# Optimization experiments

Measured on AMD Instinct MI355X. Metric: run time of the kernel, lower is better.

The kernel has to match this reference:

```python
import jax, jax.numpy as jnp
import numpy as np

EPS = 1e-5

def layer_norm(x, gamma, beta):
    mu = jnp.mean(x, axis=-1, keepdims=True)
    var = jnp.var(x, axis=-1, keepdims=True)
    return (x - mu) * jax.lax.rsqrt(var + EPS) * gamma + beta

def setup_inputs() -> dict:
    key = jax.random.key(0)
    ks = jax.random.split(key, 8)
    T, B, E, H, K = 2048, 2, 1024, 16, 64
    x = jax.random.normal(ks[0], (T, B, E), dtype=jnp.float32)
    # causal mask: 0 where allowed (s<=t), -1e9 where masked
    attn_mask = jnp.where(jnp.tril(jnp.ones((T, T), dtype=bool)), 0.0, -1e9).astype(jnp.float32)
    def xavier(k, shape, gain):
        fan_out, fan_in = shape
        std = gain * np.sqrt(2.0 / (fan_in + fan_out))
        return (jax.random.normal(k, shape, dtype=jnp.float32) * std)
    Wq = xavier(ks[1], (H * K, E), 1.0)
    Wk = xavier(ks[2], (K, E), 1.0)
    Wv = xavier(ks[3], (E, E), 1.0)
    return {
        'x': x, 'attn_mask': attn_mask,
        'Wq': Wq, 'bq': jnp.zeros((H * K,), jnp.float32),
        'Wk': Wk, 'bk': jnp.zeros((K,), jnp.float32),
        'Wv': Wv, 'bv': jnp.zeros((E,), jnp.float32),
        'k_gamma': jnp.ones((K,), jnp.float32), 'k_beta': jnp.zeros((K,), jnp.float32),
        'v_gamma': jnp.ones((E,), jnp.float32), 'v_beta': jnp.zeros((E,), jnp.float32),
    }

def reference(x, attn_mask, Wq, bq, Wk, bk, Wv, bv, k_gamma, k_beta, v_gamma, v_beta):
    T, B, E = x.shape
    K = Wk.shape[0]
    H = Wq.shape[0] // K
    q = (x @ Wq.T + bq).reshape(T, B, H, K)          # [T,B,H,K]
    k = layer_norm(x @ Wk.T + bk, k_gamma, k_beta)   # [T,B,K]
    v = layer_norm(x @ Wv.T + bv, v_gamma, v_beta)   # [T,B,E]
    # outer-product state per step, then causal cumulative sum.
    # einsum('ts,sbkd->tbkd', scaling*causal_mask, s) == cumsum over s<=t,
    # scaled per query position t by (t+1)^-0.5 (mask is causal lower-tri).
    outer = jnp.einsum('tbk,tbd->tbkd', k, v)        # [T,B,K,E]
    s = jnp.cumsum(outer, axis=0)
    scaling = jax.lax.rsqrt(jnp.arange(1, T + 1, dtype=x.dtype))
    s = s * scaling[:, None, None, None]
    qn = jnp.mean(jax.nn.softmax(q, axis=-1), axis=2)  # [T,B,K] (dropout_p=0, eval)
    attn = jnp.einsum('tbk,tbkd->tbd', qn, s)          # [T,B,E]
    return attn
```

## Files before the change

### kernel.cpp

```cpp
#include <hip/hip_runtime.h>
#include <math.h>

#define T_DIM 2048
#define B_DIM 2
#define E_DIM 1024
#define K_DIM 64
#define H_DIM 16
#define R_DIM (T_DIM * B_DIM)
#define WROWS 2176
#define NTILE 136

typedef __bf16 bf16x8 __attribute__((ext_vector_type(8)));
typedef __bf16 bf16x4 __attribute__((ext_vector_type(4)));
typedef float f32x4 __attribute__((ext_vector_type(4)));

#define GLD16(gptr, lptr)                                                      \
    __builtin_amdgcn_global_load_lds(                                          \
        (const __attribute__((address_space(1))) void*)(gptr),                 \
        (__attribute__((address_space(3))) void*)(lptr), 16, 0, 0)

__global__ __launch_bounds__(256) void cvt_all(const float* __restrict__ X,
                                               const float* __restrict__ Wq,
                                               const float* __restrict__ Wv,
                                               const float* __restrict__ Wk,
                                               __bf16* __restrict__ XB,
                                               __bf16* __restrict__ WB) {
    const size_t nq = (size_t)1024 * 1024;
    const size_t nk = (size_t)64 * 1024;
    bf16x8 o;
    if (blockIdx.x < 2048) {
        size_t g = ((size_t)blockIdx.x * 256 + threadIdx.x) * 8;
        float4 a = *(const float4*)&X[g];
        float4 b = *(const float4*)&X[g + 4];
        o[0] = (__bf16)a.x; o[1] = (__bf16)a.y; o[2] = (__bf16)a.z; o[3] = (__bf16)a.w;
        o[4] = (__bf16)b.x; o[5] = (__bf16)b.y; o[6] = (__bf16)b.z; o[7] = (__bf16)b.w;
        *(bf16x8*)&XB[g] = o;
    } else {
        size_t g = ((size_t)(blockIdx.x - 2048) * 256 + threadIdx.x) * 8;
        if (g < 2 * nq + nk) {
            const float* src;
            size_t off;
            if (g < nq)          { src = Wq; off = g; }
            else if (g < 2 * nq) { src = Wv; off = g - nq; }
            else                 { src = Wk; off = g - 2 * nq; }
            float4 a = *(const float4*)&src[off];
            float4 b = *(const float4*)&src[off + 4];
            o[0] = (__bf16)a.x; o[1] = (__bf16)a.y; o[2] = (__bf16)a.z; o[3] = (__bf16)a.w;
            o[4] = (__bf16)b.x; o[5] = (__bf16)b.y; o[6] = (__bf16)b.z; o[7] = (__bf16)b.w;
        } else {
#pragma unroll
            for (int i = 0; i < 8; ++i) o[i] = (__bf16)0.f;
        }
        *(bf16x8*)&WB[g] = o;
    }
}

__global__ __launch_bounds__(256) void gemm_mfma(const __bf16* __restrict__ XB,
                                                 const __bf16* __restrict__ WB,
                                                 const float* __restrict__ bq,
                                                 const float* __restrict__ bv,
                                                 const float* __restrict__ bk,
                                                 __bf16* __restrict__ Qb,
                                                 __bf16* __restrict__ Vb,
                                                 float* __restrict__ Kr) {
    __shared__ __bf16 Als[128 * 32];
    __shared__ __bf16 Bls[128 * 32];
    const int tid = threadIdx.x;
    const int lane = tid & 63;
    const int w = tid >> 6;
    const int wm = (w & 1) * 64;
    const int wn = (w >> 1) * 64;
    const int rBase = blockIdx.x * 128;
    const int cBase = blockIdx.y * 128;

    const int c0 = tid, c1 = tid + 256;
    const __bf16* gA0 = XB + (size_t)(rBase + (c0 >> 2)) * E_DIM + (c0 & 3) * 8;
    const __bf16* gA1 = XB + (size_t)(rBase + (c1 >> 2)) * E_DIM + (c1 & 3) * 8;
    const __bf16* gB0 = WB + (size_t)(cBase + (c0 >> 2)) * E_DIM + (c0 & 3) * 8;
    const __bf16* gB1 = WB + (size_t)(cBase + (c1 >> 2)) * E_DIM + (c1 & 3) * 8;
    __bf16* lA0 = Als + c0 * 8;
    __bf16* lA1 = Als + c1 * 8;
    __bf16* lB0 = Bls + c0 * 8;
    __bf16* lB1 = Bls + c1 * 8;

    const int fr = lane & 15;
    const int fk = (lane >> 4) * 8;
    const __bf16* aF = Als + (wm + fr) * 32 + fk;
    const __bf16* bF = Bls + (wn + fr) * 32 + fk;

    f32x4 acc[4][4] = {};

    for (int kk = 0; kk < E_DIM; kk += 32) {
        __syncthreads();
        GLD16(gA0 + kk, lA0);
        GLD16(gA1 + kk, lA1);
        GLD16(gB0 + kk, lB0);
        GLD16(gB1 + kk, lB1);
        __syncthreads();

        bf16x8 af[4], bfr[4];
#pragma unroll
        for (int mt = 0; mt < 4; ++mt) af[mt] = *(const bf16x8*)(aF + mt * 16 * 32);
#pragma unroll
        for (int nt = 0; nt < 4; ++nt) bfr[nt] = *(const bf16x8*)(bF + nt * 16 * 32);
#pragma unroll
        for (int mt = 0; mt < 4; ++mt)
#pragma unroll
            for (int nt = 0; nt < 4; ++nt)
                acc[mt][nt] = __builtin_amdgcn_mfma_f32_16x16x32_bf16(
                    af[mt], bfr[nt], acc[mt][nt], 0, 0, 0);
    }

    const int row0 = rBase + wm + (lane >> 4) * 4;
    if (cBase < 2048) {
        const float* bias;
        __bf16* Cout;
        int colBase;
        if (cBase < 1024) { bias = bq; Cout = Qb; colBase = cBase; }
        else              { bias = bv; Cout = Vb; colBase = cBase - 1024; }
        const int col0 = colBase + wn + (lane & 15);
#pragma unroll
        for (int mt = 0; mt < 4; ++mt)
#pragma unroll
            for (int nt = 0; nt < 4; ++nt) {
                int cc = col0 + nt * 16;
                float bb = bias[cc];
#pragma unroll
                for (int r = 0; r < 4; ++r)
                    Cout[(size_t)(row0 + mt * 16 + r) * E_DIM + cc] =
                        (__bf16)(acc[mt][nt][r] + bb);
            }
    } else {
        const int col0 = wn + (lane & 15);
#pragma unroll
        for (int mt = 0; mt < 4; ++mt)
#pragma unroll
            for (int nt = 0; nt < 4; ++nt) {
                int cc = col0 + nt * 16;
                if (cc < 64) {
                    float bb = bk[cc];
#pragma unroll
                    for (int r = 0; r < 4; ++r)
                        Kr[(size_t)(row0 + mt * 16 + r) * K_DIM + cc] =
                            acc[mt][nt][r] + bb;
                }
            }
    }
}

__global__ __launch_bounds__(256) void rowops(const __bf16* __restrict__ Qb,
                                              const float* __restrict__ Kraw,
                                              const __bf16* __restrict__ Vb,
                                              const float* __restrict__ kg,
                                              const float* __restrict__ kb,
                                              __bf16* __restrict__ QNB,
                                              __bf16* __restrict__ KNB,
                                              float2* __restrict__ ST) {
    const int r = blockIdx.x;
    const int tid = threadIdx.x;
    const int lane = tid & 63, wv = tid >> 6;
    const int t = r >> 1, b = r & 1;
    __shared__ float redq[4][64];
    __shared__ float redv[2][4];

    float acc = 0.f;
#pragma unroll
    for (int h4 = 0; h4 < 4; ++h4) {
        int h = wv * 4 + h4;
        float v = (float)Qb[(size_t)r * 1024 + h * 64 + lane];
        float m = v;
#pragma unroll
        for (int off = 32; off; off >>= 1) m = fmaxf(m, __shfl_xor(m, off));
        float e = expf(v - m);
        float ssum = e;
#pragma unroll
        for (int off = 32; off; off >>= 1) ssum += __shfl_xor(ssum, off);
        acc += e / ssum;
    }
    redq[wv][lane] = acc;

    {
        bf16x4 v4 = *(const bf16x4*)&Vb[(size_t)r * 1024 + tid * 4];
        float a = (float)v4[0], c = (float)v4[1], d = (float)v4[2], e = (float)v4[3];
        float s = a + c + d + e;
        float s2 = a * a + c * c + d * d + e * e;
#pragma unroll
        for (int off = 32; off; off >>= 1) {
            s += __shfl_xor(s, off);
            s2 += __shfl_xor(s2, off);
        }
        if (lane == 0) { redv[0][wv] = s; redv[1][wv] = s2; }
    }
    __syncthreads();

    if (tid < 64) {
        float s = redq[0][tid] + redq[1][tid] + redq[2][tid] + redq[3][tid];
        QNB[((size_t)b * T_DIM + t) * K_DIM + tid] = (__bf16)(s * (1.f / 16.f));
    } else if (tid < 128) {
        float v = Kraw[(size_t)r * K_DIM + lane];
        float s = v, s2 = v * v;
#pragma unroll
        for (int off = 32; off; off >>= 1) {
            s += __shfl_xor(s, off);
            s2 += __shfl_xor(s2, off);
        }
        float mean = s * (1.f / 64.f);
        float var = s2 * (1.f / 64.f) - mean * mean;
        float inv = rsqrtf(var + 1e-5f);
        KNB[((size_t)b * T_DIM + t) * K_DIM + lane] =
            (__bf16)((v - mean) * inv * kg[lane] + kb[lane]);
    } else if (tid == 128) {
        float s = redv[0][0] + redv[0][1] + redv[0][2] + redv[0][3];
        float s2 = redv[1][0] + redv[1][1] + redv[1][2] + redv[1][3];
        float mean = s * (1.f / 1024.f);
        float var = s2 * (1.f / 1024.f) - mean * mean;
        ST[r] = make_float2(mean, rsqrtf(var + 1e-5f));
    }
}

__global__ __launch_bounds__(256) void prep_score(const __bf16* __restrict__ VB,
                                                  const float2* __restrict__ ST,
                                                  const float* __restrict__ gamma,
                                                  const float* __restrict__ beta,
                                                  __bf16* __restrict__ VT,
                                                  const __bf16* __restrict__ QNB,
                                                  const __bf16* __restrict__ KNB,
                                                  __bf16* __restrict__ Pg) {
    __shared__ __align__(16) unsigned char smem[36864];
    const int bid = blockIdx.x;
    const int tid = threadIdx.x;

    if (bid < 1024) {
        float (*tile)[65] = (float(*)[65])smem;
        const int tb = bid & 31, eb = (bid >> 5) & 15, b = bid >> 9;
#pragma unroll
        for (int j = 0; j < 2; ++j) {
            int idx = tid + j * 256;
            int tl = idx >> 3, e8 = idx & 7;
            int r = (tb * 64 + tl) * B_DIM + b;
            float2 st = ST[r];
            bf16x8 v = *(const bf16x8*)&VB[(size_t)r * E_DIM + eb * 64 + e8 * 8];
#pragma unroll
            for (int i = 0; i < 8; ++i)
                tile[tl][e8 * 8 + i] = ((float)v[i] - st.x) * st.y;
        }
        __syncthreads();
#pragma unroll
        for (int j = 0; j < 4; ++j) {
            int idx = tid + j * 256;
            int e = idx >> 4, t4 = idx & 15;
            float g = gamma[eb * 64 + e], bb = beta[eb * 64 + e];
            bf16x4 o;
#pragma unroll
            for (int i = 0; i < 4; ++i) o[i] = (__bf16)(tile[t4 * 4 + i][e] * g + bb);
            *(bf16x4*)&VT[((size_t)b * E_DIM + eb * 64 + e) * T_DIM + tb * 64 + t4 * 4] = o;
        }
    } else {
        __bf16* qns = (__bf16*)smem;
        __bf16* kns = (__bf16*)(smem + 18432);
        const int idx0 = bid - 1024;
        const int b = idx0 & 1;
        const int tileId = idx0 >> 1;
        int qt = 0, rem = tileId;
        while (rem > qt) { rem -= (qt + 1); ++qt; }
        const int st = rem;
        const int lane = tid & 63;
        const int w = tid >> 6;
        const int qL = lane & 15;
        const int quad = lane >> 4;

        const __bf16* qsrc = QNB + ((size_t)b * T_DIM + qt * 128) * K_DIM;
        const __bf16* ksrc = KNB + ((size_t)b * T_DIM + st * 128) * K_DIM;
#pragma unroll
        for (int j = 0; j < 4; ++j) {
            int idx = tid + j * 256;
            int row = idx >> 3, k8 = idx & 7;
            *(bf16x8*)&qns[row * 72 + k8 * 8] = *(const bf16x8*)&qsrc[row * K_DIM + k8 * 8];
            *(bf16x8*)&kns[row * 72 + k8 * 8] = *(const bf16x8*)&ksrc[row * K_DIM + k8 * 8];
        }
        __syncthreads();

        f32x4 acc[8][2] = {};
#pragma unroll
        for (int kit = 0; kit < 2; ++kit) {
            bf16x8 bfr[2];
#pragma unroll
            for (int nt = 0; nt < 2; ++nt) {
                int q = w * 32 + nt * 16 + qL;
                bfr[nt] = *(const bf16x8*)&qns[q * 72 + kit * 32 + quad * 8];
            }
#pragma unroll
            for (int mt = 0; mt < 8; ++mt) {
                bf16x8 af = *(const bf16x8*)&kns[(mt * 16 + qL) * 72 + kit * 32 + quad * 8];
#pragma unroll
                for (int nt = 0; nt < 2; ++nt)
                    acc[mt][nt] = __builtin_amdgcn_mfma_f32_16x16x32_bf16(
                        af, bfr[nt], acc[mt][nt], 0, 0, 0);
            }
        }
        __bf16* pb = Pg + ((size_t)(b * NTILE + tileId)) * 128 * 128;
#pragma unroll
        for (int mt = 0; mt < 8; ++mt)
#pragma unroll
            for (int nt = 0; nt < 2; ++nt) {
                int q = w * 32 + nt * 16 + qL;
                int s0 = mt * 16 + quad * 4;
                bf16x4 o;
#pragma unroll
                for (int r = 0; r < 4; ++r) {
                    float val = acc[mt][nt][r];
                    if (qt == st && (s0 + r) > q) val = 0.f;
                    o[r] = (__bf16)val;
                }
                *(bf16x4*)&pb[(size_t)q * 128 + s0] = o;
            }
    }
}

__global__ __launch_bounds__(256) void flashPV(const __bf16* __restrict__ Pg,
                                               const __bf16* __restrict__ VT,
                                               float* __restrict__ OUT) {
    __shared__ __align__(16) __bf16 vts[64 * 136];
    __shared__ __align__(16) __bf16 ps[128 * 136];
    const int p = blockIdx.x;
    const int es = blockIdx.y;
    const int b = blockIdx.z;
    const int tid = threadIdx.x;
    const int lane = tid & 63;
    const int w = tid >> 6;
    const int qL = lane & 15;
    const int quad = lane >> 4;

    for (int ph = 0; ph < 2; ++ph) {
        const int qt = ph ? (15 - p) : p;
        const int tileBase = qt * (qt + 1) / 2;
        f32x4 acc[4][2] = {};

        for (int st = 0; st <= qt; ++st) {
            __syncthreads();
#pragma unroll
            for (int j = 0; j < 4; ++j) {
                int idx = tid + j * 256;
                int e = idx >> 4, sc = idx & 15;
                *(bf16x8*)&vts[e * 136 + sc * 8] =
                    *(const bf16x8*)&VT[((size_t)b * E_DIM + es * 64 + e) * T_DIM +
                                        st * 128 + sc * 8];
            }
            const __bf16* pb = Pg + ((size_t)(b * NTILE + tileBase + st)) * 128 * 128;
#pragma unroll
            for (int j = 0; j < 8; ++j) {
                int idx = tid + j * 256;
                int q = idx >> 4, sc = idx & 15;
                *(bf16x8*)&ps[q * 136 + sc * 8] = *(const bf16x8*)&pb[q * 128 + sc * 8];
            }
            __syncthreads();
#pragma unroll
            for (int kit = 0; kit < 4; ++kit) {
                bf16x8 bfr[2];
#pragma unroll
                for (int nt = 0; nt < 2; ++nt) {
                    int q = w * 32 + nt * 16 + qL;
                    bfr[nt] = *(const bf16x8*)&ps[q * 136 + kit * 32 + quad * 8];
                }
#pragma unroll
                for (int mt = 0; mt < 4; ++mt) {
                    bf16x8 af = *(const bf16x8*)&vts[(mt * 16 + qL) * 136 + kit * 32 + quad * 8];
#pragma unroll
                    for (int nt = 0; nt < 2; ++nt)
                        acc[mt][nt] = __builtin_amdgcn_mfma_f32_16x16x32_bf16(
                            af, bfr[nt], acc[mt][nt], 0, 0, 0);
                }
            }
        }
        __syncthreads();

        float* tb = (float*)vts + w * 640;
#pragma unroll
        for (int mt = 0; mt < 4; ++mt) {
#pragma unroll
            for (int nt = 0; nt < 2; ++nt)
                *(f32x4*)&tb[(nt * 16 + qL) * 20 + quad * 4] = acc[mt][nt];
#pragma unroll
            for (int j = 0; j < 2; ++j) {
                int fid = lane + j * 64;
                int q = fid >> 2, e4 = fid & 3;
                float4 val = *(const float4*)&tb[q * 20 + e4 * 4];
                int t = qt * 128 + w * 32 + q;
                float sca = rsqrtf((float)(t + 1));
                float4 r = {val.x * sca, val.y * sca, val.z * sca, val.w * sca};
                *(float4*)&OUT[((size_t)t * B_DIM + b) * E_DIM + es * 64 + mt * 16 + e4 * 4] = r;
            }
        }
    }
}

extern "C" void kernel_launch(void* const* d_in, const int* in_sizes, int n_in,
                              void* d_out, int out_size, void* d_ws,
                              size_t ws_size, hipStream_t stream) {
    const float* x = (const float*)d_in[0];
    const float* Wq = (const float*)d_in[2];
    const float* bq = (const float*)d_in[3];
    const float* Wk = (const float*)d_in[4];
    const float* bk = (const float*)d_in[5];
    const float* Wv = (const float*)d_in[6];
    const float* bv = (const float*)d_in[7];
    const float* kg = (const float*)d_in[8];
    const float* kb = (const float*)d_in[9];
    const float* vg = (const float*)d_in[10];
    const float* vb = (const float*)d_in[11];
    float* out = (float*)d_out;

    char* base = (char*)d_ws;
    const size_t MB = 1024 * 1024;
    __bf16* qb    = (__bf16*)(base + 0);
    __bf16* vbuf  = (__bf16*)(base + 8 * MB);
    float*  kraw  = (float*)(base + 16 * MB);
    __bf16* xb    = (__bf16*)(base + 17 * MB);
    __bf16* wb    = (__bf16*)(base + 25 * MB);
    __bf16* qnb   = (__bf16*)(base + 30 * MB);
    __bf16* knb   = (__bf16*)(base + 31 * MB);
    float2* stats = (float2*)(base + 32 * MB);
    __bf16* Pg  = (__bf16*)(base + 0);
    __bf16* vbT = xb;

    cvt_all<<<dim3(2048 + WROWS * 1024 / 2048), 256, 0, stream>>>(x, Wq, Wv, Wk, xb, wb);
    gemm_mfma<<<dim3(32, 17), 256, 0, stream>>>(xb, wb, bq, bv, bk, qb, vbuf, kraw);
    rowops<<<dim3(R_DIM), 256, 0, stream>>>(qb, kraw, vbuf, kg, kb, qnb, knb, stats);
    prep_score<<<dim3(1024 + 2 * NTILE), 256, 0, stream>>>(vbuf, stats, vg, vb, vbT,
                                                           qnb, knb, Pg);
    flashPV<<<dim3(8, 16, B_DIM), 256, 0, stream>>>(Pg, vbT, out);
}
```

Measured before the change: 183.6 us.

## Double-buffer GEMM LDS loads and split flashPV query-tile pairs across blocks

The projection GEMM now uses two LDS buffers, so the async global-to-LDS loads for the next k-slice are issued before computing the current one, leaving one barrier per step instead of two. flashPV no longer pairs tiles p and 15-p inside a single block. It launches one block per query tile (16×16×2 blocks), issued longest-first to improve parallelism and load balance. Risks include doubled LDS use in the GEMM, which may lower occupancy, and whether the loads actually overlap given the synchronization pattern.

```diff
diff --git a/kernel.cpp b/kernel.cpp
--- a/kernel.cpp
+++ b/kernel.cpp
@@ -63,8 +63,8 @@
                                                  __bf16* __restrict__ Qb,
                                                  __bf16* __restrict__ Vb,
                                                  float* __restrict__ Kr) {
-    __shared__ __bf16 Als[128 * 32];
-    __shared__ __bf16 Bls[128 * 32];
+    __shared__ __bf16 Als[2][128 * 32];
+    __shared__ __bf16 Bls[2][128 * 32];
     const int tid = threadIdx.x;
     const int lane = tid & 63;
     const int w = tid >> 6;
@@ -78,38 +78,61 @@
     const __bf16* gA1 = XB + (size_t)(rBase + (c1 >> 2)) * E_DIM + (c1 & 3) * 8;
     const __bf16* gB0 = WB + (size_t)(cBase + (c0 >> 2)) * E_DIM + (c0 & 3) * 8;
     const __bf16* gB1 = WB + (size_t)(cBase + (c1 >> 2)) * E_DIM + (c1 & 3) * 8;
-    __bf16* lA0 = Als + c0 * 8;
-    __bf16* lA1 = Als + c1 * 8;
-    __bf16* lB0 = Bls + c0 * 8;
-    __bf16* lB1 = Bls + c1 * 8;
+    __bf16* lA0_0 = &Als[0][c0 * 8];
+    __bf16* lA1_0 = &Als[0][c1 * 8];
+    __bf16* lB0_0 = &Bls[0][c0 * 8];
+    __bf16* lB1_0 = &Bls[0][c1 * 8];
+    __bf16* lA0_1 = &Als[1][c0 * 8];
+    __bf16* lA1_1 = &Als[1][c1 * 8];
+    __bf16* lB0_1 = &Bls[1][c0 * 8];
+    __bf16* lB1_1 = &Bls[1][c1 * 8];
 
     const int fr = lane & 15;
     const int fk = (lane >> 4) * 8;
-    const __bf16* aF = Als + (wm + fr) * 32 + fk;
-    const __bf16* bF = Bls + (wn + fr) * 32 + fk;
+    const __bf16* aF_0 = &Als[0][(wm + fr) * 32 + fk];
+    const __bf16* bF_0 = &Bls[0][(wn + fr) * 32 + fk];
+    const __bf16* aF_1 = &Als[1][(wm + fr) * 32 + fk];
+    const __bf16* bF_1 = &Bls[1][(wn + fr) * 32 + fk];
 
     f32x4 acc[4][4] = {};
 
-    for (int kk = 0; kk < E_DIM; kk += 32) {
-        __syncthreads();
-        GLD16(gA0 + kk, lA0);
-        GLD16(gA1 + kk, lA1);
-        GLD16(gB0 + kk, lB0);
-        GLD16(gB1 + kk, lB1);
-        __syncthreads();
-
-        bf16x8 af[4], bfr[4];
-#pragma unroll
-        for (int mt = 0; mt < 4; ++mt) af[mt] = *(const bf16x8*)(aF + mt * 16 * 32);
-#pragma unroll
-        for (int nt = 0; nt < 4; ++nt) bfr[nt] = *(const bf16x8*)(bF + nt * 16 * 32);
-#pragma unroll
-        for (int mt = 0; mt < 4; ++mt)
-#pragma unroll
-            for (int nt = 0; nt < 4; ++nt)
-                acc[mt][nt] = __builtin_amdgcn_mfma_f32_16x16x32_bf16(
-                    af[mt], bfr[nt], acc[mt][nt], 0, 0, 0);
-    }
+#define STAGE(B, KK)                                                           \
+    {                                                                          \
+        GLD16(gA0 + (KK), lA0_##B);                                            \
+        GLD16(gA1 + (KK), lA1_##B);                                            \
+        GLD16(gB0 + (KK), lB0_##B);                                            \
+        GLD16(gB1 + (KK), lB1_##B);                                            \
+    }
+#define COMPUTE(B)                                                             \
+    {                                                                          \
+        bf16x8 af[4], bfr[4];                                                  \
+        _Pragma("unroll") for (int mt = 0; mt < 4; ++mt)                       \
+            af[mt] = *(const bf16x8*)(aF_##B + mt * 16 * 32);                  \
+        _Pragma("unroll") for (int nt = 0; nt < 4; ++nt)                       \
+            bfr[nt] = *(const bf16x8*)(bF_##B + nt * 16 * 32);                 \
+        _Pragma("unroll") for (int mt = 0; mt < 4; ++mt)                       \
+            _Pragma("unroll") for (int nt = 0; nt < 4; ++nt)                   \
+                acc[mt][nt] = __builtin_amdgcn_mfma_f32_16x16x32_bf16(         \
+                    af[mt], bfr[nt], acc[mt][nt], 0, 0, 0);                    \
+    }
+
+    STAGE(0, 0);
+    __syncthreads();
+    STAGE(1, 32);
+    COMPUTE(0);
+    __syncthreads();
+    for (int kk = 64; kk < E_DIM; kk += 64) {
+        STAGE(0, kk);
+        COMPUTE(1);
+        __syncthreads();
+        STAGE(1, kk + 32);
+        COMPUTE(0);
+        __syncthreads();
+    }
+    COMPUTE(1);
+
+#undef STAGE
+#undef COMPUTE
 
     const int row0 = rBase + wm + (lane >> 4) * 4;
     if (cBase < 2048) {
@@ -322,7 +345,7 @@
                                                float* __restrict__ OUT) {
     __shared__ __align__(16) __bf16 vts[64 * 136];
     __shared__ __align__(16) __bf16 ps[128 * 136];
-    const int p = blockIdx.x;
+    const int qt = 15 - (int)blockIdx.x;
     const int es = blockIdx.y;
     const int b = blockIdx.z;
     const int tid = threadIdx.x;
@@ -331,65 +354,62 @@
     const int qL = lane & 15;
     const int quad = lane >> 4;
 
-    for (int ph = 0; ph < 2; ++ph) {
-        const int qt = ph ? (15 - p) : p;
-        const int tileBase = qt * (qt + 1) / 2;
-        f32x4 acc[4][2] = {};
-
-        for (int st = 0; st <= qt; ++st) {
-            __syncthreads();
-#pragma unroll
-            for (int j = 0; j < 4; ++j) {
-                int idx = tid + j * 256;
-                int e = idx >> 4, sc = idx & 15;
-                *(bf16x8*)&vts[e * 136 + sc * 8] =
-                    *(const bf16x8*)&VT[((size_t)b * E_DIM + es * 64 + e) * T_DIM +
-                                        st * 128 + sc * 8];
-            }
-            const __bf16* pb = Pg + ((size_t)(b * NTILE + tileBase + st)) * 128 * 128;
-#pragma unroll
-            for (int j = 0; j < 8; ++j) {
-                int idx = tid + j * 256;
-                int q = idx >> 4, sc = idx & 15;
-                *(bf16x8*)&ps[q * 136 + sc * 8] = *(const bf16x8*)&pb[q * 128 + sc * 8];
-            }
-            __syncthreads();
-#pragma unroll
-            for (int kit = 0; kit < 4; ++kit) {
-                bf16x8 bfr[2];
-#pragma unroll
-                for (int nt = 0; nt < 2; ++nt) {
-                    int q = w * 32 + nt * 16 + qL;
-                    bfr[nt] = *(const bf16x8*)&ps[q * 136 + kit * 32 + quad * 8];
-                }
-#pragma unroll
-                for (int mt = 0; mt < 4; ++mt) {
-                    bf16x8 af = *(const bf16x8*)&vts[(mt * 16 + qL) * 136 + kit * 32 + quad * 8];
-#pragma unroll
-                    for (int nt = 0; nt < 2; ++nt)
-                        acc[mt][nt] = __builtin_amdgcn_mfma_f32_16x16x32_bf16(
-                            af, bfr[nt], acc[mt][nt], 0, 0, 0);
-                }
-            }
-        }
-        __syncthreads();
-
-        float* tb = (float*)vts + w * 640;
-#pragma unroll
-        for (int mt = 0; mt < 4; ++mt) {
-#pragma unroll
-            for (int nt = 0; nt < 2; ++nt)
-                *(f32x4*)&tb[(nt * 16 + qL) * 20 + quad * 4] = acc[mt][nt];
-#pragma unroll
-            for (int j = 0; j < 2; ++j) {
-                int fid = lane + j * 64;
-                int q = fid >> 2, e4 = fid & 3;
-                float4 val = *(const float4*)&tb[q * 20 + e4 * 4];
-                int t = qt * 128 + w * 32 + q;
-                float sca = rsqrtf((float)(t + 1));
-                float4 r = {val.x * sca, val.y * sca, val.z * sca, val.w * sca};
-                *(float4*)&OUT[((size_t)t * B_DIM + b) * E_DIM + es * 64 + mt * 16 + e4 * 4] = r;
-            }
+    const int tileBase = qt * (qt + 1) / 2;
+    f32x4 acc[4][2] = {};
+
+    for (int st = 0; st <= qt; ++st) {
+        __syncthreads();
+#pragma unroll
+        for (int j = 0; j < 4; ++j) {
+            int idx = tid + j * 256;
+            int e = idx >> 4, sc = idx & 15;
+            *(bf16x8*)&vts[e * 136 + sc * 8] =
+                *(const bf16x8*)&VT[((size_t)b * E_DIM + es * 64 + e) * T_DIM +
+                                    st * 128 + sc * 8];
+        }
+        const __bf16* pb = Pg + ((size_t)(b * NTILE + tileBase + st)) * 128 * 128;
+#pragma unroll
+        for (int j = 0; j < 8; ++j) {
+            int idx = tid + j * 256;
+            int q = idx >> 4, sc = idx & 15;
+            *(bf16x8*)&ps[q * 136 + sc * 8] = *(const bf16x8*)&pb[q * 128 + sc * 8];
+        }
+        __syncthreads();
+#pragma unroll
+        for (int kit = 0; kit < 4; ++kit) {
+            bf16x8 bfr[2];
+#pragma unroll
+            for (int nt = 0; nt < 2; ++nt) {
+                int q = w * 32 + nt * 16 + qL;
+                bfr[nt] = *(const bf16x8*)&ps[q * 136 + kit * 32 + quad * 8];
+            }
+#pragma unroll
+            for (int mt = 0; mt < 4; ++mt) {
+                bf16x8 af = *(const bf16x8*)&vts[(mt * 16 + qL) * 136 + kit * 32 + quad * 8];
+#pragma unroll
+                for (int nt = 0; nt < 2; ++nt)
+                    acc[mt][nt] = __builtin_amdgcn_mfma_f32_16x16x32_bf16(
+                        af, bfr[nt], acc[mt][nt], 0, 0, 0);
+            }
+        }
+    }
+    __syncthreads();
+
+    float* tb = (float*)vts + w * 640;
+#pragma unroll
+    for (int mt = 0; mt < 4; ++mt) {
+#pragma unroll
+        for (int nt = 0; nt < 2; ++nt)
+            *(f32x4*)&tb[(nt * 16 + qL) * 20 + quad * 4] = acc[mt][nt];
+#pragma unroll
+        for (int j = 0; j < 2; ++j) {
+            int fid = lane + j * 64;
+            int q = fid >> 2, e4 = fid & 3;
+            float4 val = *(const float4*)&tb[q * 20 + e4 * 4];
+            int t = qt * 128 + w * 32 + q;
+            float sca = rsqrtf((float)(t + 1));
+            float4 r = {val.x * sca, val.y * sca, val.z * sca, val.w * sca};
+            *(float4*)&OUT[((size_t)t * B_DIM + b) * E_DIM + es * 64 + mt * 16 + e4 * 4] = r;
         }
     }
 }
@@ -428,5 +448,5 @@
     rowops<<<dim3(R_DIM), 256, 0, stream>>>(qb, kraw, vbuf, kg, kb, qnb, knb, stats);
     prep_score<<<dim3(1024 + 2 * NTILE), 256, 0, stream>>>(vbuf, stats, vg, vb, vbT,
                                                            qnb, knb, Pg);
-    flashPV<<<dim3(8, 16, B_DIM), 256, 0, stream>>>(Pg, vbT, out);
-}
+    flashPV<<<dim3(16, 16, B_DIM), 256, 0, stream>>>(Pg, vbT, out);
+}
```

Measured after the change: 186.4 us. No clear change (+1.5%).

## Double-buffer V tiles via async global-to-LDS loads and split flashPV grid

Applied to the files above, without the earlier changes.

flashPV now launches one block per query tile (512 blocks) instead of one block handling a balanced pair of tiles, so there are more blocks and more parallelism. V^T tiles are staged with global_load_lds into a double-buffered, XOR-swizzled LDS layout while the current tile is computed. The P tile is read directly from global memory into registers, which removes its LDS staging. In exchange, per-block work is now unbalanced across the causal triangle, and P reads depend on cache behaviour.

```diff
diff --git a/kernel.cpp b/kernel.cpp
--- a/kernel.cpp
+++ b/kernel.cpp
@@ -320,76 +320,81 @@
 __global__ __launch_bounds__(256) void flashPV(const __bf16* __restrict__ Pg,
                                                const __bf16* __restrict__ VT,
                                                float* __restrict__ OUT) {
-    __shared__ __align__(16) __bf16 vts[64 * 136];
-    __shared__ __align__(16) __bf16 ps[128 * 136];
-    const int p = blockIdx.x;
-    const int es = blockIdx.y;
-    const int b = blockIdx.z;
+    __shared__ __align__(16) __bf16 vts[2][64 * 128];
+    const int f = blockIdx.x;
+    const int p = f & 7;
+    const int r2 = f >> 3;
+    const int b = (r2 >> 1) & 1;
+    const int es = r2 >> 2;
+    const int qt = (r2 & 1) ? (15 - p) : p;
     const int tid = threadIdx.x;
     const int lane = tid & 63;
     const int w = tid >> 6;
     const int qL = lane & 15;
     const int quad = lane >> 4;
 
-    for (int ph = 0; ph < 2; ++ph) {
-        const int qt = ph ? (15 - p) : p;
-        const int tileBase = qt * (qt + 1) / 2;
-        f32x4 acc[4][2] = {};
-
-        for (int st = 0; st <= qt; ++st) {
-            __syncthreads();
-#pragma unroll
-            for (int j = 0; j < 4; ++j) {
-                int idx = tid + j * 256;
-                int e = idx >> 4, sc = idx & 15;
-                *(bf16x8*)&vts[e * 136 + sc * 8] =
-                    *(const bf16x8*)&VT[((size_t)b * E_DIM + es * 64 + e) * T_DIM +
-                                        st * 128 + sc * 8];
-            }
-            const __bf16* pb = Pg + ((size_t)(b * NTILE + tileBase + st)) * 128 * 128;
-#pragma unroll
-            for (int j = 0; j < 8; ++j) {
-                int idx = tid + j * 256;
-                int q = idx >> 4, sc = idx & 15;
-                *(bf16x8*)&ps[q * 136 + sc * 8] = *(const bf16x8*)&pb[q * 128 + sc * 8];
-            }
-            __syncthreads();
-#pragma unroll
-            for (int kit = 0; kit < 4; ++kit) {
-                bf16x8 bfr[2];
-#pragma unroll
-                for (int nt = 0; nt < 2; ++nt) {
-                    int q = w * 32 + nt * 16 + qL;
-                    bfr[nt] = *(const bf16x8*)&ps[q * 136 + kit * 32 + quad * 8];
-                }
-#pragma unroll
-                for (int mt = 0; mt < 4; ++mt) {
-                    bf16x8 af = *(const bf16x8*)&vts[(mt * 16 + qL) * 136 + kit * 32 + quad * 8];
-#pragma unroll
-                    for (int nt = 0; nt < 2; ++nt)
-                        acc[mt][nt] = __builtin_amdgcn_mfma_f32_16x16x32_bf16(
-                            af, bfr[nt], acc[mt][nt], 0, 0, 0);
-                }
-            }
-        }
+    const int tileBase = qt * (qt + 1) / 2;
+    const __bf16* vtbase = VT + ((size_t)b * E_DIM + es * 64) * T_DIM;
+    f32x4 acc[4][2] = {};
+
+#define STAGEV(BUF, ST)                                                        \
+    {                                                                          \
+        _Pragma("unroll") for (int j = 0; j < 4; ++j) {                        \
+            int idx = tid + j * 256;                                           \
+            int e = idx >> 4, scp = idx & 15;                                  \
+            int sc = scp ^ (e & 7);                                            \
+            GLD16(vtbase + (size_t)e * T_DIM + (ST) * 128 + sc * 8,            \
+                  &vts[BUF][idx * 8]);                                         \
+        }                                                                      \
+    }
+
+    STAGEV(0, 0);
+    int cur = 0;
+    for (int st = 0; st <= qt; ++st) {
+        const __bf16* pb = Pg + ((size_t)(b * NTILE + tileBase + st)) * 128 * 128;
         __syncthreads();
-
-        float* tb = (float*)vts + w * 640;
-#pragma unroll
-        for (int mt = 0; mt < 4; ++mt) {
-#pragma unroll
-            for (int nt = 0; nt < 2; ++nt)
-                *(f32x4*)&tb[(nt * 16 + qL) * 20 + quad * 4] = acc[mt][nt];
-#pragma unroll
-            for (int j = 0; j < 2; ++j) {
-                int fid = lane + j * 64;
-                int q = fid >> 2, e4 = fid & 3;
-                float4 val = *(const float4*)&tb[q * 20 + e4 * 4];
-                int t = qt * 128 + w * 32 + q;
-                float sca = rsqrtf((float)(t + 1));
-                float4 r = {val.x * sca, val.y * sca, val.z * sca, val.w * sca};
-                *(float4*)&OUT[((size_t)t * B_DIM + b) * E_DIM + es * 64 + mt * 16 + e4 * 4] = r;
-            }
+        bf16x8 pfr[4][2];
+#pragma unroll
+        for (int kit = 0; kit < 4; ++kit)
+#pragma unroll
+            for (int nt = 0; nt < 2; ++nt) {
+                int q = w * 32 + nt * 16 + qL;
+                pfr[kit][nt] = *(const bf16x8*)&pb[q * 128 + kit * 32 + quad * 8];
+            }
+        if (st < qt) STAGEV(cur ^ 1, st + 1);
+#pragma unroll
+        for (int kit = 0; kit < 4; ++kit) {
+#pragma unroll
+            for (int mt = 0; mt < 4; ++mt) {
+                int row = mt * 16 + qL;
+                int pslot = (kit * 4 + quad) ^ (row & 7);
+                bf16x8 af = *(const bf16x8*)&vts[cur][row * 128 + pslot * 8];
+#pragma unroll
+                for (int nt = 0; nt < 2; ++nt)
+                    acc[mt][nt] = __builtin_amdgcn_mfma_f32_16x16x32_bf16(
+                        af, pfr[kit][nt], acc[mt][nt], 0, 0, 0);
+            }
+        }
+        cur ^= 1;
+    }
+#undef STAGEV
+    __syncthreads();
+
+    float* tb = (float*)&vts[0][0] + w * 640;
+#pragma unroll
+    for (int mt = 0; mt < 4; ++mt) {
+#pragma unroll
+        for (int nt = 0; nt < 2; ++nt)
+            *(f32x4*)&tb[(nt * 16 + qL) * 20 + quad * 4] = acc[mt][nt];
+#pragma unroll
+        for (int j = 0; j < 2; ++j) {
+            int fid = lane + j * 64;
+            int q = fid >> 2, e4 = fid & 3;
+            float4 val = *(const float4*)&tb[q * 20 + e4 * 4];
+            int t = qt * 128 + w * 32 + q;
+            float sca = rsqrtf((float)(t + 1));
+            float4 r = {val.x * sca, val.y * sca, val.z * sca, val.w * sca};
+            *(float4*)&OUT[((size_t)t * B_DIM + b) * E_DIM + es * 64 + mt * 16 + e4 * 4] = r;
         }
     }
 }
@@ -428,5 +433,5 @@
     rowops<<<dim3(R_DIM), 256, 0, stream>>>(qb, kraw, vbuf, kg, kb, qnb, knb, stats);
     prep_score<<<dim3(1024 + 2 * NTILE), 256, 0, stream>>>(vbuf, stats, vg, vb, vbT,
                                                            qnb, knb, Pg);
-    flashPV<<<dim3(8, 16, B_DIM), 256, 0, stream>>>(Pg, vbT, out);
-}
+    flashPV<<<dim3(512), 256, 0, stream>>>(Pg, vbT, out);
+}
```

Result: slower. 188.1 us (+2.5%).

## Replace quadratic causal attention with chunked linear-attention state scan

Applied to the files above, without the earlier changes.

Replaces materializing all causal QK^T tiles followed by a flash-style P·V sweep over every prior tile with a chunked linear-attention formulation. Per-chunk K^T V states are computed, prefix-summed across 16 chunks, and each output chunk combines Q times the prefix state with an intra-chunk masked Q K^T V term. This removes the quadratic inter-chunk work and the large P buffer traffic. In exchange it adds two kernel launches and an fp32 state buffer, and stores the state as split hi/lo bf16 to preserve precision at the cost of extra MFMAs.

```diff
diff --git a/kernel.cpp b/kernel.cpp
--- a/kernel.cpp
+++ b/kernel.cpp
@@ -8,7 +8,7 @@
 #define H_DIM 16
 #define R_DIM (T_DIM * B_DIM)
 #define WROWS 2176
-#define NTILE 136
+#define NCH 16
 
 typedef __bf16 bf16x8 __attribute__((ext_vector_type(8)));
 typedef __bf16 bf16x4 __attribute__((ext_vector_type(4)));
@@ -218,178 +218,253 @@
     }
 }
 
-__global__ __launch_bounds__(256) void prep_score(const __bf16* __restrict__ VB,
-                                                  const float2* __restrict__ ST,
-                                                  const float* __restrict__ gamma,
-                                                  const float* __restrict__ beta,
-                                                  __bf16* __restrict__ VT,
-                                                  const __bf16* __restrict__ QNB,
-                                                  const __bf16* __restrict__ KNB,
-                                                  __bf16* __restrict__ Pg) {
-    __shared__ __align__(16) unsigned char smem[36864];
+__global__ __launch_bounds__(256) void prep_lnT(const __bf16* __restrict__ VB,
+                                                const float2* __restrict__ ST,
+                                                const float* __restrict__ gamma,
+                                                const float* __restrict__ beta,
+                                                __bf16* __restrict__ VT) {
+    __shared__ float tile[64][65];
     const int bid = blockIdx.x;
     const int tid = threadIdx.x;
-
-    if (bid < 1024) {
-        float (*tile)[65] = (float(*)[65])smem;
-        const int tb = bid & 31, eb = (bid >> 5) & 15, b = bid >> 9;
-#pragma unroll
-        for (int j = 0; j < 2; ++j) {
-            int idx = tid + j * 256;
-            int tl = idx >> 3, e8 = idx & 7;
-            int r = (tb * 64 + tl) * B_DIM + b;
-            float2 st = ST[r];
-            bf16x8 v = *(const bf16x8*)&VB[(size_t)r * E_DIM + eb * 64 + e8 * 8];
-#pragma unroll
-            for (int i = 0; i < 8; ++i)
-                tile[tl][e8 * 8 + i] = ((float)v[i] - st.x) * st.y;
-        }
-        __syncthreads();
-#pragma unroll
-        for (int j = 0; j < 4; ++j) {
-            int idx = tid + j * 256;
-            int e = idx >> 4, t4 = idx & 15;
-            float g = gamma[eb * 64 + e], bb = beta[eb * 64 + e];
-            bf16x4 o;
-#pragma unroll
-            for (int i = 0; i < 4; ++i) o[i] = (__bf16)(tile[t4 * 4 + i][e] * g + bb);
-            *(bf16x4*)&VT[((size_t)b * E_DIM + eb * 64 + e) * T_DIM + tb * 64 + t4 * 4] = o;
-        }
-    } else {
-        __bf16* qns = (__bf16*)smem;
-        __bf16* kns = (__bf16*)(smem + 18432);
-        const int idx0 = bid - 1024;
-        const int b = idx0 & 1;
-        const int tileId = idx0 >> 1;
-        int qt = 0, rem = tileId;
-        while (rem > qt) { rem -= (qt + 1); ++qt; }
-        const int st = rem;
-        const int lane = tid & 63;
-        const int w = tid >> 6;
-        const int qL = lane & 15;
-        const int quad = lane >> 4;
-
-        const __bf16* qsrc = QNB + ((size_t)b * T_DIM + qt * 128) * K_DIM;
-        const __bf16* ksrc = KNB + ((size_t)b * T_DIM + st * 128) * K_DIM;
-#pragma unroll
-        for (int j = 0; j < 4; ++j) {
-            int idx = tid + j * 256;
-            int row = idx >> 3, k8 = idx & 7;
-            *(bf16x8*)&qns[row * 72 + k8 * 8] = *(const bf16x8*)&qsrc[row * K_DIM + k8 * 8];
-            *(bf16x8*)&kns[row * 72 + k8 * 8] = *(const bf16x8*)&ksrc[row * K_DIM + k8 * 8];
-        }
-        __syncthreads();
-
-        f32x4 acc[8][2] = {};
-#pragma unroll
-        for (int kit = 0; kit < 2; ++kit) {
-            bf16x8 bfr[2];
-#pragma unroll
-            for (int nt = 0; nt < 2; ++nt) {
-                int q = w * 32 + nt * 16 + qL;
-                bfr[nt] = *(const bf16x8*)&qns[q * 72 + kit * 32 + quad * 8];
-            }
-#pragma unroll
-            for (int mt = 0; mt < 8; ++mt) {
-                bf16x8 af = *(const bf16x8*)&kns[(mt * 16 + qL) * 72 + kit * 32 + quad * 8];
-#pragma unroll
-                for (int nt = 0; nt < 2; ++nt)
-                    acc[mt][nt] = __builtin_amdgcn_mfma_f32_16x16x32_bf16(
-                        af, bfr[nt], acc[mt][nt], 0, 0, 0);
-            }
-        }
-        __bf16* pb = Pg + ((size_t)(b * NTILE + tileId)) * 128 * 128;
-#pragma unroll
-        for (int mt = 0; mt < 8; ++mt)
-#pragma unroll
-            for (int nt = 0; nt < 2; ++nt) {
-                int q = w * 32 + nt * 16 + qL;
-                int s0 = mt * 16 + quad * 4;
-                bf16x4 o;
-#pragma unroll
-                for (int r = 0; r < 4; ++r) {
-                    float val = acc[mt][nt][r];
-                    if (qt == st && (s0 + r) > q) val = 0.f;
-                    o[r] = (__bf16)val;
-                }
-                *(bf16x4*)&pb[(size_t)q * 128 + s0] = o;
-            }
-    }
-}
-
-__global__ __launch_bounds__(256) void flashPV(const __bf16* __restrict__ Pg,
-                                               const __bf16* __restrict__ VT,
-                                               float* __restrict__ OUT) {
-    __shared__ __align__(16) __bf16 vts[64 * 136];
-    __shared__ __align__(16) __bf16 ps[128 * 136];
-    const int p = blockIdx.x;
-    const int es = blockIdx.y;
-    const int b = blockIdx.z;
+    const int tb = bid & 31, eb = (bid >> 5) & 15, b = bid >> 9;
+#pragma unroll
+    for (int j = 0; j < 2; ++j) {
+        int idx = tid + j * 256;
+        int tl = idx >> 3, e8 = idx & 7;
+        int r = (tb * 64 + tl) * B_DIM + b;
+        float2 st = ST[r];
+        bf16x8 v = *(const bf16x8*)&VB[(size_t)r * E_DIM + eb * 64 + e8 * 8];
+#pragma unroll
+        for (int i = 0; i < 8; ++i)
+            tile[tl][e8 * 8 + i] = ((float)v[i] - st.x) * st.y;
+    }
+    __syncthreads();
+#pragma unroll
+    for (int j = 0; j < 4; ++j) {
+        int idx = tid + j * 256;
+        int e = idx >> 4, t4 = idx & 15;
+        float g = gamma[eb * 64 + e], bb = beta[eb * 64 + e];
+        bf16x4 o;
+#pragma unroll
+        for (int i = 0; i < 4; ++i) o[i] = (__bf16)(tile[t4 * 4 + i][e] * g + bb);
+        *(bf16x4*)&VT[((size_t)b * E_DIM + eb * 64 + e) * T_DIM + tb * 64 + t4 * 4] = o;
+    }
+}
+
+__global__ __launch_bounds__(256) void stateU(const __bf16* __restrict__ VT,
+                                              const __bf16* __restrict__ KNB,
+                                              float* __restrict__ U) {
+    __shared__ __bf16 Als[256 * 32];
+    __shared__ __bf16 knT[64 * 136];
+    const int c = blockIdx.x, b = blockIdx.y, eq = blockIdx.z;
     const int tid = threadIdx.x;
     const int lane = tid & 63;
     const int w = tid >> 6;
-    const int qL = lane & 15;
+    const int fr = lane & 15;
     const int quad = lane >> 4;
 
-    for (int ph = 0; ph < 2; ++ph) {
-        const int qt = ph ? (15 - p) : p;
-        const int tileBase = qt * (qt + 1) / 2;
-        f32x4 acc[4][2] = {};
-
-        for (int st = 0; st <= qt; ++st) {
-            __syncthreads();
-#pragma unroll
-            for (int j = 0; j < 4; ++j) {
-                int idx = tid + j * 256;
-                int e = idx >> 4, sc = idx & 15;
-                *(bf16x8*)&vts[e * 136 + sc * 8] =
-                    *(const bf16x8*)&VT[((size_t)b * E_DIM + es * 64 + e) * T_DIM +
-                                        st * 128 + sc * 8];
-            }
-            const __bf16* pb = Pg + ((size_t)(b * NTILE + tileBase + st)) * 128 * 128;
-#pragma unroll
-            for (int j = 0; j < 8; ++j) {
-                int idx = tid + j * 256;
-                int q = idx >> 4, sc = idx & 15;
-                *(bf16x8*)&ps[q * 136 + sc * 8] = *(const bf16x8*)&pb[q * 128 + sc * 8];
-            }
-            __syncthreads();
-#pragma unroll
-            for (int kit = 0; kit < 4; ++kit) {
-                bf16x8 bfr[2];
-#pragma unroll
-                for (int nt = 0; nt < 2; ++nt) {
-                    int q = w * 32 + nt * 16 + qL;
-                    bfr[nt] = *(const bf16x8*)&ps[q * 136 + kit * 32 + quad * 8];
+    {
+        int s = tid >> 1, kh = (tid & 1) * 32;
+        const __bf16* src = KNB + ((size_t)b * T_DIM + c * 128 + s) * K_DIM + kh;
+#pragma unroll
+        for (int i8 = 0; i8 < 4; ++i8) {
+            bf16x8 v = *(const bf16x8*)&src[i8 * 8];
+#pragma unroll
+            for (int i = 0; i < 8; ++i) knT[(kh + i8 * 8 + i) * 136 + s] = v[i];
+        }
+    }
+
+    const int e0 = eq * 256;
+    const __bf16* vtb = VT + ((size_t)b * E_DIM + e0) * T_DIM + c * 128;
+    f32x4 acc[4][4] = {};
+
+    for (int kit = 0; kit < 4; ++kit) {
+        __syncthreads();
+#pragma unroll
+        for (int j = 0; j < 4; ++j) {
+            int g = tid + j * 256;
+            int row = g >> 2, part = g & 3;
+            GLD16(vtb + (size_t)row * T_DIM + kit * 32 + part * 8, &Als[g * 8]);
+        }
+        __syncthreads();
+        bf16x8 af[4], bfr[4];
+#pragma unroll
+        for (int mt = 0; mt < 4; ++mt)
+            af[mt] = *(const bf16x8*)&Als[(w * 64 + mt * 16 + fr) * 32 + quad * 8];
+#pragma unroll
+        for (int nt = 0; nt < 4; ++nt)
+            bfr[nt] = *(const bf16x8*)&knT[(nt * 16 + fr) * 136 + kit * 32 + quad * 8];
+#pragma unroll
+        for (int mt = 0; mt < 4; ++mt)
+#pragma unroll
+            for (int nt = 0; nt < 4; ++nt)
+                acc[mt][nt] = __builtin_amdgcn_mfma_f32_16x16x32_bf16(
+                    af[mt], bfr[nt], acc[mt][nt], 0, 0, 0);
+    }
+
+    float* ub = U + ((size_t)(c * 2 + b) * 1024 + e0) * K_DIM;
+#pragma unroll
+    for (int mt = 0; mt < 4; ++mt)
+#pragma unroll
+        for (int nt = 0; nt < 4; ++nt) {
+            int k = nt * 16 + fr;
+#pragma unroll
+            for (int r = 0; r < 4; ++r)
+                ub[(size_t)(w * 64 + mt * 16 + quad * 4 + r) * K_DIM + k] =
+                    acc[mt][nt][r];
+        }
+}
+
+__global__ __launch_bounds__(256) void scanS(const float* __restrict__ U,
+                                             __bf16* __restrict__ Shi,
+                                             __bf16* __restrict__ Slo) {
+    const size_t idx = (size_t)blockIdx.x * 256 + threadIdx.x;
+    float run = 0.f;
+#pragma unroll
+    for (int c = 0; c < NCH; ++c) {
+        __bf16 h = (__bf16)run;
+        Shi[(size_t)c * 131072 + idx] = h;
+        Slo[(size_t)c * 131072 + idx] = (__bf16)(run - (float)h);
+        run += U[(size_t)c * 131072 + idx];
+    }
+}
+
+__global__ __launch_bounds__(256) void outPV(const __bf16* __restrict__ QNB,
+                                             const __bf16* __restrict__ KNB,
+                                             const __bf16* __restrict__ VT,
+                                             const __bf16* __restrict__ Shi,
+                                             const __bf16* __restrict__ Slo,
+                                             float* __restrict__ OUT) {
+    __shared__ __align__(16) __bf16 qns[128 * 72];
+    __shared__ __align__(16) __bf16 Pl[128 * 136];
+    __shared__ __align__(16) __bf16 Vls[128 * 32];
+    const int c = blockIdx.x, b = blockIdx.y, eo = blockIdx.z;
+    const int tid = threadIdx.x;
+    const int lane = tid & 63;
+    const int w = tid >> 6;
+    const int fr = lane & 15;
+    const int quad = lane >> 4;
+
+#pragma unroll
+    for (int j = 0; j < 4; ++j) {
+        int idx = tid + j * 256;
+        int row = idx >> 3, k8 = idx & 7;
+        *(bf16x8*)&qns[row * 72 + k8 * 8] =
+            *(const bf16x8*)&QNB[((size_t)b * T_DIM + c * 128 + row) * K_DIM + k8 * 8];
+    }
+    __syncthreads();
+
+    const __bf16* knc = KNB + ((size_t)b * T_DIM + c * 128) * K_DIM;
+    {
+        f32x4 pacc[8][2] = {};
+#pragma unroll
+        for (int kit = 0; kit < 2; ++kit) {
+            bf16x8 bq[2];
+#pragma unroll
+            for (int nt = 0; nt < 2; ++nt) {
+                int q = w * 32 + nt * 16 + fr;
+                bq[nt] = *(const bf16x8*)&qns[q * 72 + kit * 32 + quad * 8];
+            }
+#pragma unroll
+            for (int mt = 0; mt < 8; ++mt) {
+                bf16x8 af = *(const bf16x8*)&knc[(size_t)(mt * 16 + fr) * K_DIM +
+                                                 kit * 32 + quad * 8];
+#pragma unroll
+                for (int nt = 0; nt < 2; ++nt)
+                    pacc[mt][nt] = __builtin_amdgcn_mfma_f32_16x16x32_bf16(
+                        af, bq[nt], pacc[mt][nt], 0, 0, 0);
+            }
+        }
+#pragma unroll
+        for (int mt = 0; mt < 8; ++mt)
+#pragma unroll
+            for (int nt = 0; nt < 2; ++nt) {
+                int q = w * 32 + nt * 16 + fr;
+                int s0 = mt * 16 + quad * 4;
+                bf16x4 o;
+#pragma unroll
+                for (int r = 0; r < 4; ++r) {
+                    float val = pacc[mt][nt][r];
+                    if (s0 + r > q) val = 0.f;
+                    o[r] = (__bf16)val;
                 }
-#pragma unroll
-                for (int mt = 0; mt < 4; ++mt) {
-                    bf16x8 af = *(const bf16x8*)&vts[(mt * 16 + qL) * 136 + kit * 32 + quad * 8];
-#pragma unroll
-                    for (int nt = 0; nt < 2; ++nt)
-                        acc[mt][nt] = __builtin_amdgcn_mfma_f32_16x16x32_bf16(
-                            af, bfr[nt], acc[mt][nt], 0, 0, 0);
+                *(bf16x4*)&Pl[q * 136 + s0] = o;
+            }
+    }
+    __syncthreads();
+
+    const int we = (w & 1) * 64, wt = (w >> 1) * 64;
+    const int e0 = eo * 128;
+    f32x4 acc[4][4] = {};
+
+    if (c > 0) {
+        const __bf16* sh = Shi + (size_t)c * 131072 + ((size_t)b * 1024 + e0 + we) * K_DIM;
+        const __bf16* sl = Slo + (size_t)c * 131072 + ((size_t)b * 1024 + e0 + we) * K_DIM;
+#pragma unroll
+        for (int kit = 0; kit < 2; ++kit) {
+            bf16x8 bq[4];
+#pragma unroll
+            for (int nt = 0; nt < 4; ++nt) {
+                int t = wt + nt * 16 + fr;
+                bq[nt] = *(const bf16x8*)&qns[t * 72 + kit * 32 + quad * 8];
+            }
+#pragma unroll
+            for (int mt = 0; mt < 4; ++mt) {
+                size_t ro = (size_t)(mt * 16 + fr) * K_DIM + kit * 32 + quad * 8;
+                bf16x8 ah = *(const bf16x8*)&sh[ro];
+                bf16x8 al = *(const bf16x8*)&sl[ro];
+#pragma unroll
+                for (int nt = 0; nt < 4; ++nt) {
+                    acc[mt][nt] = __builtin_amdgcn_mfma_f32_16x16x32_bf16(
+                        ah, bq[nt], acc[mt][nt], 0, 0, 0);
+                    acc[mt][nt] = __builtin_amdgcn_mfma_f32_16x16x32_bf16(
+                        al, bq[nt], acc[mt][nt], 0, 0, 0);
                 }
             }
         }
+    }
+
+    const __bf16* vtb = VT + ((size_t)b * E_DIM + e0) * T_DIM + c * 128;
+    for (int kit = 0; kit < 4; ++kit) {
         __syncthreads();
-
-        float* tb = (float*)vts + w * 640;
-#pragma unroll
-        for (int mt = 0; mt < 4; ++mt) {
-#pragma unroll
-            for (int nt = 0; nt < 2; ++nt)
-                *(f32x4*)&tb[(nt * 16 + qL) * 20 + quad * 4] = acc[mt][nt];
-#pragma unroll
-            for (int j = 0; j < 2; ++j) {
-                int fid = lane + j * 64;
-                int q = fid >> 2, e4 = fid & 3;
-                float4 val = *(const float4*)&tb[q * 20 + e4 * 4];
-                int t = qt * 128 + w * 32 + q;
-                float sca = rsqrtf((float)(t + 1));
-                float4 r = {val.x * sca, val.y * sca, val.z * sca, val.w * sca};
-                *(float4*)&OUT[((size_t)t * B_DIM + b) * E_DIM + es * 64 + mt * 16 + e4 * 4] = r;
-            }
+#pragma unroll
+        for (int j = 0; j < 2; ++j) {
+            int g = tid + j * 256;
+            int row = g >> 2, part = g & 3;
+            GLD16(vtb + (size_t)row * T_DIM + kit * 32 + part * 8, &Vls[g * 8]);
+        }
+        __syncthreads();
+        bf16x8 av[4], bp[4];
+#pragma unroll
+        for (int mt = 0; mt < 4; ++mt)
+            av[mt] = *(const bf16x8*)&Vls[(we + mt * 16 + fr) * 32 + quad * 8];
+#pragma unroll
+        for (int nt = 0; nt < 4; ++nt)
+            bp[nt] = *(const bf16x8*)&Pl[(wt + nt * 16 + fr) * 136 + kit * 32 + quad * 8];
+#pragma unroll
+        for (int mt = 0; mt < 4; ++mt)
+#pragma unroll
+            for (int nt = 0; nt < 4; ++nt)
+                acc[mt][nt] = __builtin_amdgcn_mfma_f32_16x16x32_bf16(
+                    av[mt], bp[nt], acc[mt][nt], 0, 0, 0);
+    }
+    __syncthreads();
+
+    float* tb = (float*)qns + w * 1280;
+#pragma unroll
+    for (int mt = 0; mt < 4; ++mt) {
+#pragma unroll
+        for (int nt = 0; nt < 4; ++nt)
+            *(f32x4*)&tb[(nt * 16 + fr) * 20 + quad * 4] = acc[mt][nt];
+#pragma unroll
+        for (int j = 0; j < 4; ++j) {
+            int fid = lane + j * 64;
+            int trow = fid >> 2, e4 = fid & 3;
+            float4 val = *(const float4*)&tb[trow * 20 + e4 * 4];
+            int t = c * 128 + wt + trow;
+            float sca = rsqrtf((float)(t + 1));
+            float4 r = {val.x * sca, val.y * sca, val.z * sca, val.w * sca};
+            *(float4*)&OUT[((size_t)t * B_DIM + b) * E_DIM + e0 + we + mt * 16 + e4 * 4] = r;
         }
     }
 }
@@ -420,13 +495,16 @@
     __bf16* qnb   = (__bf16*)(base + 30 * MB);
     __bf16* knb   = (__bf16*)(base + 31 * MB);
     float2* stats = (float2*)(base + 32 * MB);
-    __bf16* Pg  = (__bf16*)(base + 0);
-    __bf16* vbT = xb;
+    float*  Ubuf = (float*)(base + 0);
+    __bf16* Shi  = (__bf16*)(base + 8 * MB);
+    __bf16* Slo  = (__bf16*)(base + 12 * MB);
+    __bf16* vbT  = xb;
 
     cvt_all<<<dim3(2048 + WROWS * 1024 / 2048), 256, 0, stream>>>(x, Wq, Wv, Wk, xb, wb);
     gemm_mfma<<<dim3(32, 17), 256, 0, stream>>>(xb, wb, bq, bv, bk, qb, vbuf, kraw);
     rowops<<<dim3(R_DIM), 256, 0, stream>>>(qb, kraw, vbuf, kg, kb, qnb, knb, stats);
-    prep_score<<<dim3(1024 + 2 * NTILE), 256, 0, stream>>>(vbuf, stats, vg, vb, vbT,
-                                                           qnb, knb, Pg);
-    flashPV<<<dim3(8, 16, B_DIM), 256, 0, stream>>>(Pg, vbT, out);
-}
+    prep_lnT<<<dim3(1024), 256, 0, stream>>>(vbuf, stats, vg, vb, vbT);
+    stateU<<<dim3(NCH, 2, 4), 256, 0, stream>>>(vbT, knb, Ubuf);
+    scanS<<<dim3(512), 256, 0, stream>>>(Ubuf, Shi, Slo);
+    outPV<<<dim3(NCH, 2, 8), 256, 0, stream>>>(qnb, knb, vbT, Shi, Slo, out);
+}
```

Result: faster. 175.3 us (-4.5%).
